# Kernel tuning notes

Hardware: AMD Instinct MI355X
Metric: run time of the kernel (lower is better)

## Reference

```python
import jax, jax.numpy as jnp
import numpy as np

TEMP = 20.0     # args.temp
ATT_WT = 0.3    # args.att_wt
EPS = 1e-12     # torch F.normalize eps

L, B, C, H, W = 3, 2, 2048, 60, 60   # 3 layer4 bottleneck maps
CH = 256                              # merged feature channels for f_q/f_s


def setup_inputs() -> dict:
    key = jax.random.key(0)
    k1, k2, k3, k4, k5 = jax.random.split(key, 5)
    return {
        "fq_feats": jax.random.normal(k1, (L, B, C, H, W), dtype=jnp.float32),
        "fs_feats": jax.random.normal(k2, (L, B, C, H, W), dtype=jnp.float32),
        "f_q": jax.random.normal(k3, (B, CH, H, W), dtype=jnp.float32),
        "f_s": jax.random.normal(k4, (B, CH, H, W), dtype=jnp.float32),
        "corr_weight": jax.random.normal(k5, (L,), dtype=jnp.float32),
    }


def _l2_normalize(x, axis):
    # torch F.normalize(dim=1): x / max(||x||, eps)
    n = jnp.sqrt(jnp.sum(x * x, axis=axis, keepdims=True))
    return x / jnp.maximum(n, EPS)


def reference(fq_feats, fs_feats, f_q, f_s, corr_weight):
    b, ch, h, w = f_q.shape
    hw = h * w
    # per-scale channel-wise L2 normalize (cosine correlation)
    fqn = _l2_normalize(fq_feats, axis=2)   # [L,B,C,H,W]
    fsn = _l2_normalize(fs_feats, axis=2)
    # get_corr: pairwise cosine similarity volume per scale -> [B, L, hw_q, hw_s]
    fq_flat = fqn.reshape(fqn.shape[0], b, fqn.shape[2], hw)  # [L,B,C,hw]
    fs_flat = fsn.reshape(fsn.shape[0], b, fsn.shape[2], hw)
    corr = jnp.einsum('lbcq,lbcs->blqs', fq_flat, fs_flat)    # [B,L,hw,hw]
    # MatchNet corr_forward: 1x1 conv reducing match_ch -> 1, softmax over
    # support positions (scaled by temp), attend into v = f_s
    red = jnp.einsum('l,blqs->bqs', corr_weight, corr)        # [B,hw,hw]
    attn = jax.nn.softmax(red * TEMP, axis=-1)                # over support hw
    v = f_s.reshape(b, ch, hw)                                # [B,ch,hw]
    att_fq = jnp.einsum('bqs,bcs->bcq', attn, v).reshape(b, ch, h, w)
    fq = (f_q + att_fq * ATT_WT) / (1.0 + ATT_WT)
    return fq, att_fq
```

## Files before the change

kernel.cpp:

```cpp
#include <hip/hip_runtime.h>
#include <hip/hip_bf16.h>
#include <stdint.h>

#define L3D 3
#define BD 2
#define CD 2048
#define HW 3600
#define CH 256
#define HWP 3712
#define KD 6144
#define SP 3712
#define SP2 3840
#define LB6 6
#define NPLANE 12
#define NT 48

typedef __attribute__((ext_vector_type(8))) short short8;
typedef __attribute__((ext_vector_type(4))) float f32x4;
typedef __attribute__((ext_vector_type(4))) int i32x4;
typedef __attribute__((ext_vector_type(8))) int i32x8;

__device__ __forceinline__ short f2bf(float v) {
  uint32_t x = __float_as_uint(v);
  uint32_t r = (x + 0x7FFFu + ((x >> 16) & 1u)) >> 16;
  return (short)(r & 0xFFFFu);
}

__device__ __forceinline__ float bf2f(short s) {
  return __uint_as_float(((uint32_t)(uint16_t)s) << 16);
}

__device__ __forceinline__ void load_lds16(const void* g, void* l) {
  __builtin_amdgcn_global_load_lds(
      (const __attribute__((address_space(1))) void*)g,
      (__attribute__((address_space(3))) void*)l, 16, 0, 0);
}

__global__ __launch_bounds__(256) void norm_k(const float* __restrict__ fq,
                                              const float* __restrict__ fs,
                                              float* __restrict__ part) {
  const int qt = blockIdx.x * 256;
  const int j = blockIdx.y;
  const int cs = blockIdx.z;
  const bool isq = (j < LB6);
  const int lb = isq ? j : j - LB6;
  const float* x = (isq ? fq : fs) + (size_t)lb * CD * HW;

  const int tid = threadIdx.x;
  const int qg = tid & 63;
  const int cp = tid >> 6;
  const int q4 = qt + qg * 4;

  f32x4 a0 = (f32x4){0.f, 0.f, 0.f, 0.f};
  f32x4 a1 = a0, a2 = a0, a3 = a0;
  if (q4 < HW) {
    const float* p = x + ((size_t)cs * 256 + cp) * HW + q4;
    for (int i = 0; i < 64; i += 4) {
      f32x4 v0 = *reinterpret_cast<const f32x4*>(p + (size_t)(i + 0) * 4 * HW);
      f32x4 v1 = *reinterpret_cast<const f32x4*>(p + (size_t)(i + 1) * 4 * HW);
      f32x4 v2 = *reinterpret_cast<const f32x4*>(p + (size_t)(i + 2) * 4 * HW);
      f32x4 v3 = *reinterpret_cast<const f32x4*>(p + (size_t)(i + 3) * 4 * HW);
      a0 += v0 * v0; a1 += v1 * v1; a2 += v2 * v2; a3 += v3 * v3;
    }
  }
  f32x4 a = (a0 + a1) + (a2 + a3);

  __shared__ float rb[4][256];
  *reinterpret_cast<f32x4*>(&rb[cp][qg * 4]) = a;
  __syncthreads();
  float s = rb[0][tid] + rb[1][tid] + rb[2][tid] + rb[3][tid];
  part[((size_t)cs * NPLANE + j) * SP2 + qt + tid] = s;
}

__global__ __launch_bounds__(256) void trans_k(const float* __restrict__ fq,
                                               const float* __restrict__ fs,
                                               const float* __restrict__ cw,
                                               const float* __restrict__ part,
                                               uint8_t* __restrict__ An,
                                               uint8_t* __restrict__ Bn) {
  const int j = blockIdx.y;
  const int qt = blockIdx.x * 64;
  const int cg = blockIdx.z;
  const bool isq = (j < LB6);
  const int lb = isq ? j : j - LB6;
  const int l = lb / BD, b = lb % BD;
  const float* x = (isq ? fq : fs) + (size_t)lb * CD * HW;
  uint8_t* dst = isq ? An : Bn;

  const int tid = threadIdx.x;

  __shared__ float ivs[64];
  if (tid < 64) {
    const int q = qt + tid;
    float s = 0.f;
#pragma unroll
    for (int cs = 0; cs < 8; cs++) s += part[((size_t)cs * NPLANE + j) * SP2 + q];
    const float scale = isq ? (cw[l] * 32.0f) : 32.0f;
    ivs[tid] = (1.f / fmaxf(sqrtf(s), 1e-12f)) * scale;
  }

  __shared__ float tile[64][65];
  const int tx = tid & 63, partid = tid >> 6;
  const int q = qt + tx;
  const int wx = tid & 7, wy = tid >> 3;

  for (int t = 0; t < 8; t++) {
    const int ct = cg * 8 + t;
    const float* px = x + (size_t)ct * 64 * HW;
    __syncthreads();
#pragma unroll
    for (int r = 0; r < 16; r++) {
      int cl = r * 4 + partid;
      tile[cl][tx] = (q < HW) ? px[(size_t)cl * HW + q] : 0.f;
    }
    __syncthreads();
#pragma unroll
    for (int it = 0; it < 2; it++) {
      int qrow = wy + it * 32;
      int qq = qt + qrow;
      if (qq < HW) {
        float iv = ivs[qrow];
        float v[8];
#pragma unroll
        for (int jj = 0; jj < 8; jj++) v[jj] = tile[wx * 8 + jj][qrow] * iv;
        int lo = 0, hi = 0;
        lo = __builtin_amdgcn_cvt_pk_fp8_f32(v[0], v[1], lo, false);
        lo = __builtin_amdgcn_cvt_pk_fp8_f32(v[2], v[3], lo, true);
        hi = __builtin_amdgcn_cvt_pk_fp8_f32(v[4], v[5], hi, false);
        hi = __builtin_amdgcn_cvt_pk_fp8_f32(v[6], v[7], hi, true);
        int2 pk = make_int2(lo, hi);
        *reinterpret_cast<int2*>(dst + ((size_t)b * HWP + qq) * KD +
                                 (size_t)l * CD + ct * 64 + wx * 8) = pk;
      }
    }
  }
}

__global__ __launch_bounds__(512, 2) void gemm_main(const uint8_t* __restrict__ A,
                                                    const uint8_t* __restrict__ B,
                                                    __hip_bfloat16* __restrict__ C) {
  const int bz = blockIdx.y;
  const int lin = blockIdx.x;
  const int m_t = lin / 15, n_t = lin % 15;
  const int m0 = m_t * 256, n0 = n_t * 256;
  const int tid = threadIdx.x;
  const int lane = tid & 63;
  const int wv = tid >> 6;

  __shared__ uint8_t lA[2][256 * 128];
  __shared__ uint8_t lB[2][256 * 128];

  const uint8_t* gA = A + (size_t)bz * HWP * KD;
  const uint8_t* gB = B + (size_t)bz * HWP * KD;

  const int r_loc = tid >> 3;
  const int slot = tid & 7;
  const int csw = (slot - r_loc) & 7;
  const int wavebase = (tid & ~63) * 16;

  const int wr = (wv >> 2) * 128;
  const int wc = (wv & 3) * 64;
  const int ml = lane & 15;
  const int kg = lane >> 4;

  f32x4 acc[8][4];
#pragma unroll
  for (int i = 0; i < 8; i++)
#pragma unroll
    for (int jj = 0; jj < 4; jj++) acc[i][jj] = (f32x4){0.f, 0.f, 0.f, 0.f};

  auto stage = [&](int t, int bufi) {
    const int k0 = t * 128;
#pragma unroll
    for (int i = 0; i < 4; i++) {
      load_lds16(gA + (size_t)(m0 + i * 64 + r_loc) * KD + k0 + csw * 16,
                 &lA[bufi][i * 8192 + wavebase]);
      load_lds16(gB + (size_t)(n0 + i * 64 + r_loc) * KD + k0 + csw * 16,
                 &lB[bufi][i * 8192 + wavebase]);
    }
  };

  auto rdfrag = [&](const uint8_t* base, int row) -> i32x8 {
    const uint8_t* rp = base + (row << 7);
    i32x4 lo = *reinterpret_cast<const i32x4*>(rp + (((kg * 2)     + row) & 7) * 16);
    i32x4 hi = *reinterpret_cast<const i32x4*>(rp + (((kg * 2 + 1) + row) & 7) * 16);
    return __builtin_shufflevector(lo, hi, 0, 1, 2, 3, 4, 5, 6, 7);
  };

  stage(0, 0);
  asm volatile("s_waitcnt vmcnt(0)" ::: "memory");
  __builtin_amdgcn_s_barrier();

  for (int t = 0; t < NT; t++) {
    const int cur = t & 1;
    const uint8_t* pA = lA[cur];
    const uint8_t* pB = lB[cur];
    const bool st = (t + 1 < NT);
    i32x8 af[4], bfr[4];

#pragma unroll
    for (int x = 0; x < 4; x++) af[x] = rdfrag(pA, wr + x * 16 + ml);
#pragma unroll
    for (int x = 0; x < 2; x++) bfr[x] = rdfrag(pB, wc + x * 16 + ml);
    if (st) stage(t + 1, cur ^ 1);
    __builtin_amdgcn_s_barrier();
    asm volatile("s_waitcnt lgkmcnt(0)");
    __builtin_amdgcn_s_setprio(1);
#pragma unroll
    for (int mt = 0; mt < 4; mt++)
#pragma unroll
      for (int nt = 0; nt < 2; nt++)
        acc[mt][nt] = __builtin_amdgcn_mfma_scale_f32_16x16x128_f8f6f4(
            af[mt], bfr[nt], acc[mt][nt], 0, 0, 0, 0x7F7F7F7F, 0, 0x7F7F7F7F);
    __builtin_amdgcn_s_setprio(0);
    __builtin_amdgcn_s_barrier();

#pragma unroll
    for (int x = 2; x < 4; x++) bfr[x] = rdfrag(pB, wc + x * 16 + ml);
    __builtin_amdgcn_s_barrier();
    asm volatile("s_waitcnt lgkmcnt(0)");
    __builtin_amdgcn_s_setprio(1);
#pragma unroll
    for (int mt = 0; mt < 4; mt++)
#pragma unroll
      for (int nt = 2; nt < 4; nt++)
        acc[mt][nt] = __builtin_amdgcn_mfma_scale_f32_16x16x128_f8f6f4(
            af[mt], bfr[nt], acc[mt][nt], 0, 0, 0, 0x7F7F7F7F, 0, 0x7F7F7F7F);
    __builtin_amdgcn_s_setprio(0);
    __builtin_amdgcn_s_barrier();

#pragma unroll
    for (int x = 0; x < 4; x++) af[x] = rdfrag(pA, wr + 64 + x * 16 + ml);
    __builtin_amdgcn_s_barrier();
    asm volatile("s_waitcnt lgkmcnt(0)");
    __builtin_amdgcn_s_setprio(1);
#pragma unroll
    for (int mt = 0; mt < 4; mt++)
#pragma unroll
      for (int nt = 2; nt < 4; nt++)
        acc[4 + mt][nt] = __builtin_amdgcn_mfma_scale_f32_16x16x128_f8f6f4(
            af[mt], bfr[nt], acc[4 + mt][nt], 0, 0, 0, 0x7F7F7F7F, 0, 0x7F7F7F7F);
    __builtin_amdgcn_s_setprio(0);
    __builtin_amdgcn_s_barrier();

    __builtin_amdgcn_s_barrier();
    __builtin_amdgcn_s_setprio(1);
#pragma unroll
    for (int mt = 0; mt < 4; mt++)
#pragma unroll
      for (int nt = 0; nt < 2; nt++)
        acc[4 + mt][nt] = __builtin_amdgcn_mfma_scale_f32_16x16x128_f8f6f4(
            af[mt], bfr[nt], acc[4 + mt][nt], 0, 0, 0, 0x7F7F7F7F, 0, 0x7F7F7F7F);
    __builtin_amdgcn_s_setprio(0);
    if (st) asm volatile("s_waitcnt vmcnt(0)" ::: "memory");
    __builtin_amdgcn_s_barrier();
  }

  __hip_bfloat16* oc = C + (size_t)bz * HWP * SP;
  const int rq = (lane >> 4) * 4;
  const int cl = lane & 15;
#pragma unroll
  for (int mt = 0; mt < 8; mt++) {
    const int rb = m0 + wr + mt * 16 + rq;
#pragma unroll
    for (int nt = 0; nt < 4; nt++) {
      const int col = n0 + wc + nt * 16 + cl;
      if (col < SP) {
        f32x4 v = acc[mt][nt];
#pragma unroll
        for (int r = 0; r < 4; r++) {
          const int rr = rb + r;
          if (rr < HW) *reinterpret_cast<short*>(&oc[(size_t)rr * SP + col]) = f2bf(v[r]);
        }
      }
    }
  }
}

__global__ __launch_bounds__(256) void softmax_k(const __hip_bfloat16* __restrict__ red,
                                                 __hip_bfloat16* __restrict__ attn) {
  const int q = blockIdx.x;
  const int b = blockIdx.y;
  const __hip_bfloat16* row = red + ((size_t)b * HWP + q) * SP;
  __hip_bfloat16* orow = attn + ((size_t)b * HWP + q) * SP;
  const int tid = threadIdx.x;
  const int lane = tid & 63, wv = tid >> 6;
  const float SM = 20.0f / 1024.0f;

  float v0[8], v1[8];
  const int c1 = 256 + tid;
  const bool has1 = (c1 < 450);

  float mx = -3.4e38f;
  {
    short8 pk = *reinterpret_cast<const short8*>(&row[(size_t)tid * 8]);
#pragma unroll
    for (int j = 0; j < 8; j++) { v0[j] = bf2f(pk[j]); mx = fmaxf(mx, v0[j]); }
  }
  if (has1) {
    short8 pk = *reinterpret_cast<const short8*>(&row[(size_t)c1 * 8]);
#pragma unroll
    for (int j = 0; j < 8; j++) { v1[j] = bf2f(pk[j]); mx = fmaxf(mx, v1[j]); }
  }
  for (int off = 32; off > 0; off >>= 1) mx = fmaxf(mx, __shfl_down(mx, off, 64));
  __shared__ float sm[4];
  if (lane == 0) sm[wv] = mx;
  __syncthreads();
  mx = fmaxf(fmaxf(sm[0], sm[1]), fmaxf(sm[2], sm[3]));

  float sum = 0.f;
#pragma unroll
  for (int j = 0; j < 8; j++) { float e = __expf((v0[j] - mx) * SM); v0[j] = e; sum += e; }
  if (has1) {
#pragma unroll
    for (int j = 0; j < 8; j++) { float e = __expf((v1[j] - mx) * SM); v1[j] = e; sum += e; }
  }
  for (int off = 32; off > 0; off >>= 1) sum += __shfl_down(sum, off, 64);
  __syncthreads();
  if (lane == 0) sm[wv] = sum;
  __syncthreads();
  const float inv = 1.f / (sm[0] + sm[1] + sm[2] + sm[3]);

  {
    short8 o;
#pragma unroll
    for (int j = 0; j < 8; j++) o[j] = f2bf(v0[j] * inv);
    *reinterpret_cast<short8*>(&orow[(size_t)tid * 8]) = o;
  }
  if (has1) {
    short8 o;
#pragma unroll
    for (int j = 0; j < 8; j++) o[j] = f2bf(v1[j] * inv);
    *reinterpret_cast<short8*>(&orow[(size_t)c1 * 8]) = o;
  } else if (c1 < 464) {
    short8 z = {0, 0, 0, 0, 0, 0, 0, 0};
    *reinterpret_cast<short8*>(&orow[(size_t)c1 * 8]) = z;
  }
}

__global__ __launch_bounds__(256) void castv_k(const float* __restrict__ fs,
                                               __hip_bfloat16* __restrict__ vb) {
  const int idx = blockIdx.x * 256 + threadIdx.x;
  if (idx >= BD * CH * SP) return;
  const int s = idx % SP;
  const int bc = idx / SP;
  float v = (s < HW) ? fs[(size_t)bc * HW + s] : 0.f;
  *reinterpret_cast<short*>(&vb[idx]) = f2bf(v);
}

__global__ __launch_bounds__(256, 2) void pv_gemm(const __hip_bfloat16* __restrict__ A,
                                                  const __hip_bfloat16* __restrict__ B,
                                                  const float* __restrict__ fqin,
                                                  float* __restrict__ out) {
  const int bz = blockIdx.z;
  const int m0 = blockIdx.y * 128;
  const int n0 = blockIdx.x * 64;
  const int tid = threadIdx.x;
  const int lane = tid & 63;
  const int wv = tid >> 6;

  __shared__ __hip_bfloat16 lA[128 * 32];
  __shared__ __hip_bfloat16 lB[64 * 32];

  const __hip_bfloat16* gA = A + (size_t)bz * CH * SP;
  const __hip_bfloat16* gB = B + (size_t)bz * HWP * SP;

  const int r0 = tid >> 2;
  const int kc = (tid & 3) * 8;
  const int wb = (tid & ~63) * 8;

  const int wr = (wv >> 1) * 64;
  const int wc = (wv & 1) * 32;
  const int ml = lane & 15;
  const int kq = (lane >> 4) * 8;

  f32x4 acc[4][2];
#pragma unroll
  for (int i = 0; i < 4; i++)
#pragma unroll
    for (int jj = 0; jj < 2; jj++) acc[i][jj] = (f32x4){0.f, 0.f, 0.f, 0.f};

  for (int k0 = 0; k0 < SP; k0 += 32) {
    const __hip_bfloat16* pa0 = gA + (size_t)(m0 + r0) * SP + k0 + kc;
    const __hip_bfloat16* pb0 = gB + (size_t)(n0 + r0) * SP + k0 + kc;
    load_lds16(pa0, &lA[wb]);
    load_lds16(pa0 + (size_t)64 * SP, &lA[wb + 2048]);
    load_lds16(pb0, &lB[wb]);
    __syncthreads();

    short8 af[4], bfr[2];
#pragma unroll
    for (int t = 0; t < 4; t++)
      af[t] = *reinterpret_cast<const short8*>(&lA[(wr + t * 16 + ml) * 32 + kq]);
#pragma unroll
    for (int t = 0; t < 2; t++)
      bfr[t] = *reinterpret_cast<const short8*>(&lB[(wc + t * 16 + ml) * 32 + kq]);
#pragma unroll
    for (int mt = 0; mt < 4; mt++)
#pragma unroll
      for (int nt = 0; nt < 2; nt++)
        acc[mt][nt] = __builtin_amdgcn_mfma_f32_16x16x32_bf16(af[mt], bfr[nt], acc[mt][nt], 0, 0, 0);
    __syncthreads();
  }

  const size_t obase = (size_t)bz * CH * HW;
  const size_t attoff = (size_t)BD * CH * HW;
  const int rq = (lane >> 4) * 4;
  const int cl = lane & 15;
#pragma unroll
  for (int mt = 0; mt < 4; mt++) {
    const int rb = m0 + wr + mt * 16 + rq;
#pragma unroll
    for (int nt = 0; nt < 2; nt++) {
      const int col = n0 + wc + nt * 16 + cl;
      if (col < HW) {
        f32x4 v = acc[mt][nt];
#pragma unroll
        for (int r = 0; r < 4; r++) {
          const int c = rb + r;
          size_t oi = obase + (size_t)c * HW + col;
          float att = v[r];
          out[oi] = (fqin[oi] + 0.3f * att) * (1.0f / 1.3f);
          out[attoff + oi] = att;
        }
      }
    }
  }
}

extern "C" void kernel_launch(void* const* d_in, const int* in_sizes, int n_in,
                              void* d_out, int out_size, void* d_ws, size_t ws_size,
                              hipStream_t stream) {
  const float* fqf = (const float*)d_in[0];
  const float* fsf = (const float*)d_in[1];
  const float* f_q = (const float*)d_in[2];
  const float* f_s = (const float*)d_in[3];
  const float* cw  = (const float*)d_in[4];
  float* out = (float*)d_out;

  char* w = (char*)d_ws;
  uint8_t* An = (uint8_t*)w;   w += (size_t)BD * HWP * KD;
  uint8_t* Bn = (uint8_t*)w;   w += (size_t)BD * HWP * KD;
  __hip_bfloat16* red = (__hip_bfloat16*)w;  w += (size_t)BD * HWP * SP * 2;
  float* part = (float*)w;
  __hip_bfloat16* attn = (__hip_bfloat16*)An;
  __hip_bfloat16* vb = (__hip_bfloat16*)(An + (size_t)BD * HWP * SP * 2);
  (void)ws_size; (void)in_sizes; (void)n_in; (void)out_size;

  norm_k<<<dim3(15, NPLANE, 8), 256, 0, stream>>>(fqf, fsf, part);
  trans_k<<<dim3(57, NPLANE, 4), 256, 0, stream>>>(fqf, fsf, cw, part, An, Bn);
  gemm_main<<<dim3(225, BD), 512, 0, stream>>>(An, Bn, red);
  softmax_k<<<dim3(HW, BD), 256, 0, stream>>>(red, attn);
  castv_k<<<(BD * CH * SP + 255) / 256, 256, 0, stream>>>(f_s, vb);
  pv_gemm<<<dim3(58, 2, BD), 256, 0, stream>>>(vb, attn, f_q, out);
}
```

Baseline: 809.1 us.

## Interleave prefetch in FP8 GEMM, XCD-remap blocks, double-buffer PV GEMM

The main FP8 correlation GEMM now spreads its next-tile global-to-LDS loads across the MFMA phases and issues part of tile t+2 early, with partial vmcnt waits in place of one bulk stage and full drain. Its grid is flattened to one dimension and remapped so consecutive tiles land on the same XCD, which should improve L2 reuse. The PV bf16 GEMM moves from a single-buffered K=32 loop with two syncthreads per step to double-buffered K=64 byte-swizzled tiles. The aim is to hide load latency and cut barrier overhead, at the cost of more LDS use and delicate waitcnt accounting.

New measurement: 800.7 us. Within noise of the previous version (-1.0%).

```diff
diff --git a/kernel.cpp b/kernel.cpp
--- a/kernel.cpp
+++ b/kernel.cpp
@@ -14,6 +14,7 @@
 #define LB6 6
 #define NPLANE 12
 #define NT 48
+#define PVNT 58
 
 typedef __attribute__((ext_vector_type(8))) short short8;
 typedef __attribute__((ext_vector_type(4))) float f32x4;
@@ -139,8 +140,11 @@
 __global__ __launch_bounds__(512, 2) void gemm_main(const uint8_t* __restrict__ A,
                                                     const uint8_t* __restrict__ B,
                                                     __hip_bfloat16* __restrict__ C) {
-  const int bz = blockIdx.y;
-  const int lin = blockIdx.x;
+  const int orig = blockIdx.x;
+  const int xcd = orig & 7, idx = orig >> 3;
+  const int wg = (xcd < 2 ? xcd * 57 : 114 + (xcd - 2) * 56) + idx;
+  const int bz = wg / 225;
+  const int lin = wg % 225;
   const int m_t = lin / 15, n_t = lin % 15;
   const int m0 = m_t * 256, n0 = n_t * 256;
   const int tid = threadIdx.x;
@@ -169,15 +173,13 @@
 #pragma unroll
     for (int jj = 0; jj < 4; jj++) acc[i][jj] = (f32x4){0.f, 0.f, 0.f, 0.f};
 
-  auto stage = [&](int t, int bufi) {
-    const int k0 = t * 128;
-#pragma unroll
-    for (int i = 0; i < 4; i++) {
-      load_lds16(gA + (size_t)(m0 + i * 64 + r_loc) * KD + k0 + csw * 16,
-                 &lA[bufi][i * 8192 + wavebase]);
-      load_lds16(gB + (size_t)(n0 + i * 64 + r_loc) * KD + k0 + csw * 16,
-                 &lB[bufi][i * 8192 + wavebase]);
-    }
+  auto stA = [&](int t, int bufi, int i) {
+    load_lds16(gA + (size_t)(m0 + i * 64 + r_loc) * KD + t * 128 + csw * 16,
+               &lA[bufi][i * 8192 + wavebase]);
+  };
+  auto stB = [&](int t, int bufi, int i) {
+    load_lds16(gB + (size_t)(n0 + i * 64 + r_loc) * KD + t * 128 + csw * 16,
+               &lB[bufi][i * 8192 + wavebase]);
   };
 
   auto rdfrag = [&](const uint8_t* base, int row) -> i32x8 {
@@ -187,22 +189,26 @@
     return __builtin_shufflevector(lo, hi, 0, 1, 2, 3, 4, 5, 6, 7);
   };
 
-  stage(0, 0);
-  asm volatile("s_waitcnt vmcnt(0)" ::: "memory");
+  stA(0, 0, 0); stA(0, 0, 1); stA(0, 0, 2); stA(0, 0, 3);
+  stB(0, 0, 0); stB(0, 0, 1); stB(0, 0, 2); stB(0, 0, 3);
+  stA(1, 1, 0); stA(1, 1, 1);
+  asm volatile("s_waitcnt vmcnt(2)" ::: "memory");
   __builtin_amdgcn_s_barrier();
 
   for (int t = 0; t < NT; t++) {
     const int cur = t & 1;
+    const int nxt = cur ^ 1;
     const uint8_t* pA = lA[cur];
     const uint8_t* pB = lB[cur];
-    const bool st = (t + 1 < NT);
+    const bool s1 = (t + 1 < NT);
+    const bool s2 = (t + 2 < NT);
     i32x8 af[4], bfr[4];
 
 #pragma unroll
     for (int x = 0; x < 4; x++) af[x] = rdfrag(pA, wr + x * 16 + ml);
 #pragma unroll
     for (int x = 0; x < 2; x++) bfr[x] = rdfrag(pB, wc + x * 16 + ml);
-    if (st) stage(t + 1, cur ^ 1);
+    if (s1) { stA(t + 1, nxt, 2); stA(t + 1, nxt, 3); }
     __builtin_amdgcn_s_barrier();
     asm volatile("s_waitcnt lgkmcnt(0)");
     __builtin_amdgcn_s_setprio(1);
@@ -217,6 +223,7 @@
 
 #pragma unroll
     for (int x = 2; x < 4; x++) bfr[x] = rdfrag(pB, wc + x * 16 + ml);
+    if (s1) { stB(t + 1, nxt, 0); stB(t + 1, nxt, 1); }
     __builtin_amdgcn_s_barrier();
     asm volatile("s_waitcnt lgkmcnt(0)");
     __builtin_amdgcn_s_setprio(1);
@@ -231,6 +238,7 @@
 
 #pragma unroll
     for (int x = 0; x < 4; x++) af[x] = rdfrag(pA, wr + 64 + x * 16 + ml);
+    if (s1) { stB(t + 1, nxt, 2); stB(t + 1, nxt, 3); }
     __builtin_amdgcn_s_barrier();
     asm volatile("s_waitcnt lgkmcnt(0)");
     __builtin_amdgcn_s_setprio(1);
@@ -243,6 +251,7 @@
     __builtin_amdgcn_s_setprio(0);
     __builtin_amdgcn_s_barrier();
 
+    if (s2) { stA(t + 2, cur, 0); stA(t + 2, cur, 1); }
     __builtin_amdgcn_s_barrier();
     __builtin_amdgcn_s_setprio(1);
 #pragma unroll
@@ -252,7 +261,8 @@
         acc[4 + mt][nt] = __builtin_amdgcn_mfma_scale_f32_16x16x128_f8f6f4(
             af[mt], bfr[nt], acc[4 + mt][nt], 0, 0, 0, 0x7F7F7F7F, 0, 0x7F7F7F7F);
     __builtin_amdgcn_s_setprio(0);
-    if (st) asm volatile("s_waitcnt vmcnt(0)" ::: "memory");
+    if (s2)      asm volatile("s_waitcnt vmcnt(2)" ::: "memory");
+    else if (s1) asm volatile("s_waitcnt vmcnt(0)" ::: "memory");
     __builtin_amdgcn_s_barrier();
   }
 
@@ -359,20 +369,21 @@
   const int lane = tid & 63;
   const int wv = tid >> 6;
 
-  __shared__ __hip_bfloat16 lA[128 * 32];
-  __shared__ __hip_bfloat16 lB[64 * 32];
-
-  const __hip_bfloat16* gA = A + (size_t)bz * CH * SP;
-  const __hip_bfloat16* gB = B + (size_t)bz * HWP * SP;
-
-  const int r0 = tid >> 2;
-  const int kc = (tid & 3) * 8;
-  const int wb = (tid & ~63) * 8;
+  __shared__ uint8_t lA[2][128 * 128];
+  __shared__ uint8_t lB[2][64 * 128];
+
+  const uint8_t* gA = (const uint8_t*)(A + (size_t)bz * CH * SP);
+  const uint8_t* gB = (const uint8_t*)(B + (size_t)bz * HWP * SP);
+
+  const int r2 = tid >> 3;
+  const int slot = tid & 7;
+  const int csw = (slot - r2) & 7;
+  const int wb16 = (tid & ~63) * 16;
 
   const int wr = (wv >> 1) * 64;
   const int wc = (wv & 1) * 32;
   const int ml = lane & 15;
-  const int kq = (lane >> 4) * 8;
+  const int kg = lane >> 4;
 
   f32x4 acc[4][2];
 #pragma unroll
@@ -380,27 +391,54 @@
 #pragma unroll
     for (int jj = 0; jj < 2; jj++) acc[i][jj] = (f32x4){0.f, 0.f, 0.f, 0.f};
 
-  for (int k0 = 0; k0 < SP; k0 += 32) {
-    const __hip_bfloat16* pa0 = gA + (size_t)(m0 + r0) * SP + k0 + kc;
-    const __hip_bfloat16* pb0 = gB + (size_t)(n0 + r0) * SP + k0 + kc;
-    load_lds16(pa0, &lA[wb]);
-    load_lds16(pa0 + (size_t)64 * SP, &lA[wb + 2048]);
-    load_lds16(pb0, &lB[wb]);
-    __syncthreads();
-
-    short8 af[4], bfr[2];
-#pragma unroll
-    for (int t = 0; t < 4; t++)
-      af[t] = *reinterpret_cast<const short8*>(&lA[(wr + t * 16 + ml) * 32 + kq]);
-#pragma unroll
-    for (int t = 0; t < 2; t++)
-      bfr[t] = *reinterpret_cast<const short8*>(&lB[(wc + t * 16 + ml) * 32 + kq]);
-#pragma unroll
-    for (int mt = 0; mt < 4; mt++)
-#pragma unroll
-      for (int nt = 0; nt < 2; nt++)
-        acc[mt][nt] = __builtin_amdgcn_mfma_f32_16x16x32_bf16(af[mt], bfr[nt], acc[mt][nt], 0, 0, 0);
-    __syncthreads();
+  auto stA = [&](int t, int bufi, int i) {
+    load_lds16(gA + (size_t)(m0 + i * 32 + r2) * (SP * 2) + t * 128 + csw * 16,
+               &lA[bufi][i * 4096 + wb16]);
+  };
+  auto stB = [&](int t, int bufi, int i) {
+    load_lds16(gB + (size_t)(n0 + i * 32 + r2) * (SP * 2) + t * 128 + csw * 16,
+               &lB[bufi][i * 4096 + wb16]);
+  };
+
+  auto rdf = [&](const uint8_t* base, int r, int s) -> short8 {
+    return *reinterpret_cast<const short8*>(
+        base + (r << 7) + (((s * 4 + kg) + r) & 7) * 16);
+  };
+
+  stA(0, 0, 0); stA(0, 0, 1); stA(0, 0, 2); stA(0, 0, 3);
+  stB(0, 0, 0); stB(0, 0, 1);
+  asm volatile("s_waitcnt vmcnt(0)" ::: "memory");
+  __builtin_amdgcn_s_barrier();
+
+  for (int t = 0; t < PVNT; t++) {
+    const int cur = t & 1;
+    const int nxt = cur ^ 1;
+    const bool s1 = (t + 1 < PVNT);
+    if (s1) {
+      stA(t + 1, nxt, 0); stA(t + 1, nxt, 1); stA(t + 1, nxt, 2); stA(t + 1, nxt, 3);
+      stB(t + 1, nxt, 0); stB(t + 1, nxt, 1);
+    }
+    const uint8_t* pA = lA[cur];
+    const uint8_t* pB = lB[cur];
+    short8 af[2][4], bq[2][2];
+#pragma unroll
+    for (int s = 0; s < 2; s++) {
+#pragma unroll
+      for (int mt = 0; mt < 4; mt++) af[s][mt] = rdf(pA, wr + mt * 16 + ml, s);
+#pragma unroll
+      for (int nt = 0; nt < 2; nt++) bq[s][nt] = rdf(pB, wc + nt * 16 + ml, s);
+    }
+    asm volatile("s_waitcnt lgkmcnt(0)");
+#pragma unroll
+    for (int s = 0; s < 2; s++)
+#pragma unroll
+      for (int mt = 0; mt < 4; mt++)
+#pragma unroll
+        for (int nt = 0; nt < 2; nt++)
+          acc[mt][nt] = __builtin_amdgcn_mfma_f32_16x16x32_bf16(
+              af[s][mt], bq[s][nt], acc[mt][nt], 0, 0, 0);
+    if (s1) asm volatile("s_waitcnt vmcnt(0)" ::: "memory");
+    __builtin_amdgcn_s_barrier();
   }
 
   const size_t obase = (size_t)bz * CH * HW;
@@ -449,7 +487,7 @@
 
   norm_k<<<dim3(15, NPLANE, 8), 256, 0, stream>>>(fqf, fsf, part);
   trans_k<<<dim3(57, NPLANE, 4), 256, 0, stream>>>(fqf, fsf, cw, part, An, Bn);
-  gemm_main<<<dim3(225, BD), 512, 0, stream>>>(An, Bn, red);
+  gemm_main<<<dim3(450), 512, 0, stream>>>(An, Bn, red);
   softmax_k<<<dim3(HW, BD), 256, 0, stream>>>(red, attn);
   castv_k<<<(BD * CH * SP + 255) / 256, 256, 0, stream>>>(f_s, vb);
   pv_gemm<<<dim3(58, 2, BD), 256, 0, stream>>>(vb, attn, f_q, out);
```
